# Kernel optimization log

Measured on AMD Instinct MI355X. Metric: run time of the kernel, lower is better.

Reference implementation:

```python
import jax, jax.numpy as jnp
import numpy as np

H = 4096          # hidden_size
I = 14336         # intermediate_size
SC = int(0.3 * I) # beta * I -> size of cached x_topk (4300)
HC = int(0.05 * I)# gamma * I -> helper top-k count (716)


def setup_inputs() -> dict:
    key = jax.random.key(0)
    ks = jax.random.split(key, 7)
    s = 0.02
    return {
        "x": jax.random.normal(ks[0], (1, 1, H), dtype=jnp.float32),
        "x_topk": jax.random.randint(ks[1], (SC,), 0, I, dtype=jnp.int64),
        "gate_w": jax.random.normal(ks[2], (I, H), dtype=jnp.float32) * s,
        "up_w": jax.random.normal(ks[3], (I, H), dtype=jnp.float32) * s,
        "down_w": jax.random.normal(ks[4], (H, I), dtype=jnp.float32) * s,
        "helper_w1": jax.random.normal(ks[5], (1024, H), dtype=jnp.float32) * s,
        "helper_w2": jax.random.normal(ks[6], (I, 1024), dtype=jnp.float32) * s,
    }


def reference(x, x_topk, gate_w, up_w, down_w, helper_w1, helper_w2):
    # --- sparsity predictor (SimpleLinearModel): two bias-free linears ---
    h = (x @ helper_w1.T) @ helper_w2.T                       # [1,1,I]
    up_mask_index = jax.lax.top_k(h.reshape(-1), HC)[1]       # [HC]

    # --- combine cached core indices with predicted indices, dedup ---
    combined = jnp.concatenate([x_topk.astype(jnp.int32),
                                up_mask_index.astype(jnp.int32)])  # [SC+HC]
    K = combined.shape[0]
    uniq = jnp.unique(combined, size=K, fill_value=I)         # padded with I
    valid = (uniq < I)                                        # [K] bool
    idx = jnp.where(valid, uniq, 0)                           # safe gather idx

    # --- gather weight rows/columns, reduced gated-MLP matmul ---
    gate_f = gate_w[idx]                                      # [K,H]
    up_f = up_w[idx]                                          # [K,H]
    gate_out = jnp.einsum('bsh,kh->bsk', x, gate_f)           # [1,1,K]
    up_out = jnp.einsum('bsh,kh->bsk', x, up_f)               # [1,1,K]
    tv = jax.nn.silu(gate_out) * up_out                       # act_fn = SiLU
    tv = tv * valid.astype(tv.dtype)                          # zero padded dups

    down_f = down_w[:, idx]                                   # [H,K]
    down_value = jnp.einsum('bsk,hk->bsh', tv, down_f)        # [1,1,H]
    return down_value
```

## Files before the change

### kernel.cpp

```cpp
#include <hip/hip_runtime.h>
#include <math.h>

#define H_DIM 4096
#define I_DIM 14336
#define HB_DIM 1024
#define SC_K 4300
#define HC_K 716

typedef float floatx4 __attribute__((ext_vector_type(4)));

__device__ __forceinline__ unsigned sortable(float f) {
    unsigned u = __float_as_uint(f);
    return (u & 0x80000000u) ? ~u : (u | 0x80000000u);
}

__device__ __forceinline__ floatx4 ntload4(const float* p) {
    return __builtin_nontemporal_load((const floatx4*)p);
}

__device__ __forceinline__ void compute_tv_row(const float* __restrict__ x,
                                               const float* __restrict__ gate_w,
                                               const float* __restrict__ up_w,
                                               float* __restrict__ tv, int row, int lane) {
    const float* gr = gate_w + (size_t)row * H_DIM;
    const float* ur = up_w + (size_t)row * H_DIM;
    float gs = 0.f, us = 0.f;
#pragma unroll 4
    for (int c = 0; c < H_DIM; c += 256) {
        int cc = c + lane * 4;
        float4 xv = *(const float4*)(x + cc);
        floatx4 g = ntload4(gr + cc);
        floatx4 u = ntload4(ur + cc);
        gs += g.x * xv.x + g.y * xv.y + g.z * xv.z + g.w * xv.w;
        us += u.x * xv.x + u.y * xv.y + u.z * xv.z + u.w * xv.w;
    }
#pragma unroll
    for (int o = 32; o >= 1; o >>= 1) {
        gs += __shfl_xor(gs, o);
        us += __shfl_xor(us, o);
    }
    if (lane == 0) {
        float s = gs / (1.f + expf(-gs));
        tv[row] = s * us;
    }
}

__global__ __launch_bounds__(256) void k1_h1(
    const float* __restrict__ x, const float* __restrict__ hw1,
    float* __restrict__ h1) {
    int wid = threadIdx.x >> 6, lane = threadIdx.x & 63;
    int row = blockIdx.x * 4 + wid;
    const float* mr = hw1 + (size_t)row * H_DIM;
    float s = 0.f;
#pragma unroll 4
    for (int c = 0; c < H_DIM; c += 256) {
        int cc = c + lane * 4;
        floatx4 m = ntload4(mr + cc);
        float4 v = *(const float4*)(x + cc);
        s += m.x * v.x + m.y * v.y + m.z * v.z + m.w * v.w;
    }
#pragma unroll
    for (int o = 32; o >= 1; o >>= 1) s += __shfl_xor(s, o);
    if (lane == 0) h1[row] = s;
}

__global__ __launch_bounds__(256) void k2_h_gateup(
    const float* __restrict__ h1, const float* __restrict__ hw2,
    float* __restrict__ hbuf, const int* __restrict__ x_topk,
    const float* __restrict__ x, const float* __restrict__ gate_w,
    const float* __restrict__ up_w, float* __restrict__ tv) {
    int wid = threadIdx.x >> 6, lane = threadIdx.x & 63;
    int b = blockIdx.x;
    if (b < I_DIM / 4) {
        int row = b * 4 + wid;
        const float* mr = hw2 + (size_t)row * HB_DIM;
        float s = 0.f;
#pragma unroll
        for (int c = 0; c < HB_DIM; c += 256) {
            int cc = c + lane * 4;
            floatx4 m = ntload4(mr + cc);
            float4 v = *(const float4*)(h1 + cc);
            s += m.x * v.x + m.y * v.y + m.z * v.z + m.w * v.w;
        }
#pragma unroll
        for (int o = 32; o >= 1; o >>= 1) s += __shfl_xor(s, o);
        if (lane == 0) hbuf[row] = s;
    } else {
        int row = (b - I_DIM / 4) * 4 + wid;
        bool found = false;
        for (int k = lane; k < SC_K; k += 64) found |= (x_topk[k] == row);
        if (__any(found)) compute_tv_row(x, gate_w, up_w, tv, row, lane);
    }
}

__global__ __launch_bounds__(1024) void select_kernel(
    const float* __restrict__ h, const int* __restrict__ x_topk,
    float* __restrict__ tv, int* __restrict__ rlist, int* __restrict__ rcount) {
    __shared__ unsigned hist[16][256];
    __shared__ unsigned wpart[4];
    __shared__ unsigned bitT[448], bitS[448];
    __shared__ int s_d, s_above, s_tie_cnt, s_rc;
    __shared__ int tie_idx[2048];
    int tid = threadIdx.x;
    int lane = tid & 63, wid = tid >> 6;

    unsigned key[14];
#pragma unroll
    for (int j = 0; j < 14; ++j) key[j] = sortable(h[j * 1024 + tid]);

    if (tid < 448) { bitT[tid] = 0; bitS[tid] = 0; }
    if (tid == 0) { s_tie_cnt = 0; s_rc = 0; }
    __syncthreads();

    for (int k = tid; k < SC_K; k += 1024) {
        int idx = x_topk[k];
        if ((unsigned)idx < (unsigned)I_DIM) atomicOr(&bitT[idx >> 5], 1u << (idx & 31));
    }

    unsigned prefix = 0;
    int above = 0;

    for (int p = 0; p < 4; ++p) {
        int s = 24 - 8 * p;
        {
            unsigned* hp = &hist[0][0];
            for (int i = tid; i < 4096; i += 1024) hp[i] = 0;
        }
        __syncthreads();
#pragma unroll
        for (int j = 0; j < 14; ++j) {
            unsigned u = key[j];
            bool in_sub = (p == 0) || ((u >> (s + 8)) == (prefix >> (s + 8)));
            if (in_sub) atomicAdd(&hist[wid][(u >> s) & 0xFF], 1u);
        }
        __syncthreads();
        unsigned cnt = 0, incl = 0;
        if (tid < 256) {
#pragma unroll
            for (int w = 0; w < 16; ++w) cnt += hist[w][tid];
        }
        incl = cnt;
#pragma unroll
        for (int o = 1; o < 64; o <<= 1) {
            unsigned v = __shfl_up(incl, o);
            if (lane >= o) incl += v;
        }
        if (tid < 256 && lane == 63) wpart[wid] = incl;
        __syncthreads();
        if (tid < 256) {
            unsigned add = 0;
            for (int w2 = 0; w2 < wid; ++w2) add += wpart[w2];
            incl += add;
            unsigned total = wpart[0] + wpart[1] + wpart[2] + wpart[3];
            unsigned suf = total - incl;
            unsigned needk = (unsigned)(HC_K - above);
            if (suf < needk && suf + cnt >= needk) {
                s_d = tid;
                s_above = above + (int)suf;
            }
        }
        __syncthreads();
        prefix |= ((unsigned)s_d) << s;
        above = s_above;
        __syncthreads();
    }

    unsigned T = prefix;
    int need2 = HC_K - above;

#pragma unroll
    for (int j = 0; j < 14; ++j) {
        unsigned u = key[j];
        int i = j * 1024 + tid;
        if (u > T) atomicOr(&bitS[i >> 5], 1u << (i & 31));
        else if (u == T) {
            int pp = atomicAdd(&s_tie_cnt, 1);
            if (pp < 2048) tie_idx[pp] = i;
        }
    }
    __syncthreads();
    int C = s_tie_cnt;
    if (C <= 2048) {
        for (int m = tid; m < C; m += 1024) {
            int my = tie_idx[m];
            int rank = 0;
            for (int j = 0; j < C; ++j) rank += (tie_idx[j] < my) ? 1 : 0;
            if (rank < need2) atomicOr(&bitS[my >> 5], 1u << (my & 31));
        }
    } else if (tid == 0) {
        int left = need2;
        for (int i = 0; i < I_DIM && left > 0; ++i)
            if (sortable(h[i]) == T) { atomicOr(&bitS[i >> 5], 1u << (i & 31)); --left; }
    }
    __syncthreads();

#pragma unroll
    for (int j = 0; j < 14; ++j) {
        int i = j * 1024 + tid;
        bool t = (bitT[i >> 5] >> (i & 31)) & 1u;
        bool sl = (bitS[i >> 5] >> (i & 31)) & 1u;
        if (!t) {
            if (sl) {
                int pp = atomicAdd(&s_rc, 1);
                rlist[pp] = i;
            } else {
                tv[i] = 0.f;
            }
        }
    }
    __syncthreads();
    if (tid == 0) *rcount = s_rc;
}

__global__ __launch_bounds__(256) void k3_residual(
    const float* __restrict__ x, const float* __restrict__ gate_w,
    const float* __restrict__ up_w, const int* __restrict__ rlist,
    const int* __restrict__ rcount, float* __restrict__ tv) {
    int wid = threadIdx.x >> 6, lane = threadIdx.x & 63;
    int gw = blockIdx.x * 4 + wid;
    if (gw < *rcount) compute_tv_row(x, gate_w, up_w, tv, rlist[gw], lane);
}

__global__ __launch_bounds__(256) void k4_down(
    const float* __restrict__ tv, const float* __restrict__ down_w,
    float* __restrict__ out) {
    int wid = threadIdx.x >> 6, lane = threadIdx.x & 63;
    int row = blockIdx.x * 4 + wid;
    const float* mr = down_w + (size_t)row * I_DIM;
    float s = 0.f;
#pragma unroll 4
    for (int c = 0; c < I_DIM; c += 256) {
        int cc = c + lane * 4;
        floatx4 m = ntload4(mr + cc);
        float4 v = *(const float4*)(tv + cc);
        s += m.x * v.x + m.y * v.y + m.z * v.z + m.w * v.w;
    }
#pragma unroll
    for (int o = 32; o >= 1; o >>= 1) s += __shfl_xor(s, o);
    if (lane == 0) out[row] = s;
}

extern "C" void kernel_launch(void* const* d_in, const int* in_sizes, int n_in,
                              void* d_out, int out_size, void* d_ws, size_t ws_size,
                              hipStream_t stream) {
    const float* x      = (const float*)d_in[0];
    const int*   x_topk = (const int*)d_in[1];
    const float* gate_w = (const float*)d_in[2];
    const float* up_w   = (const float*)d_in[3];
    const float* down_w = (const float*)d_in[4];
    const float* hw1    = (const float*)d_in[5];
    const float* hw2    = (const float*)d_in[6];
    float* out = (float*)d_out;

    float* ws    = (float*)d_ws;
    float* h1    = ws;
    float* hbuf  = ws + 1024;
    float* tv    = ws + 1024 + I_DIM;
    int*   rlist = (int*)(ws + 1024 + 2 * I_DIM);
    int*   rcount = rlist + 768;

    k1_h1<<<HB_DIM / 4, 256, 0, stream>>>(x, hw1, h1);
    k2_h_gateup<<<2 * (I_DIM / 4), 256, 0, stream>>>(h1, hw2, hbuf, x_topk, x,
                                                     gate_w, up_w, tv);
    select_kernel<<<1, 1024, 0, stream>>>(hbuf, x_topk, tv, rlist, rcount);
    k3_residual<<<(HC_K + 3) / 4, 256, 0, stream>>>(x, gate_w, up_w, rlist, rcount, tv);
    k4_down<<<H_DIM / 4, 256, 0, stream>>>(tv, down_w, out);
}
```

Measured before the change: 114.7 us.

## Map gate/up waves directly to cached indices instead of scanning x_topk per row

The fused helper/gate-up kernel now gives one wave to each x_topk entry and computes that row directly. Before, every one of the I rows scanned all 4300 cached indices to test membership. Fourteen extra blocks build a per-1024-row bitmap in shared memory and zero tv for rows not in the cached set. The select kernel no longer keeps a selection bitmap or does a final zeroing pass: it appends non-cached top-k rows to the residual list directly, and the histogram rows are padded to 257 entries to reduce bank conflicts. Duplicate entries in x_topk now cause the same row to be computed twice with identical results, which is redundant work but a benign race.

```diff
diff --git a/kernel.cpp b/kernel.cpp
--- a/kernel.cpp
+++ b/kernel.cpp
@@ -64,13 +64,13 @@
     if (lane == 0) h1[row] = s;
 }
 
-__global__ __launch_bounds__(256) void k2_h_gateup(
+__global__ __launch_bounds__(256) void k2_mix(
     const float* __restrict__ h1, const float* __restrict__ hw2,
     float* __restrict__ hbuf, const int* __restrict__ x_topk,
     const float* __restrict__ x, const float* __restrict__ gate_w,
     const float* __restrict__ up_w, float* __restrict__ tv) {
-    int wid = threadIdx.x >> 6, lane = threadIdx.x & 63;
     int b = blockIdx.x;
+    int wid = threadIdx.x >> 6, lane = threadIdx.x & 63;
     if (b < I_DIM / 4) {
         int row = b * 4 + wid;
         const float* mr = hw2 + (size_t)row * HB_DIM;
@@ -85,20 +85,36 @@
 #pragma unroll
         for (int o = 32; o >= 1; o >>= 1) s += __shfl_xor(s, o);
         if (lane == 0) hbuf[row] = s;
+    } else if (b < I_DIM / 4 + (SC_K + 3) / 4) {
+        int gw = (b - I_DIM / 4) * 4 + wid;
+        if (gw < SC_K) {
+            int idx = x_topk[gw];
+            if ((unsigned)idx < (unsigned)I_DIM)
+                compute_tv_row(x, gate_w, up_w, tv, idx, lane);
+        }
     } else {
-        int row = (b - I_DIM / 4) * 4 + wid;
-        bool found = false;
-        for (int k = lane; k < SC_K; k += 64) found |= (x_topk[k] == row);
-        if (__any(found)) compute_tv_row(x, gate_w, up_w, tv, row, lane);
+        int zb = b - (I_DIM / 4 + (SC_K + 3) / 4);
+        int base = zb * 1024;
+        __shared__ unsigned bits[32];
+        if (threadIdx.x < 32) bits[threadIdx.x] = 0;
+        __syncthreads();
+        for (int k = threadIdx.x; k < SC_K; k += 256) {
+            int idx = x_topk[k] - base;
+            if ((unsigned)idx < 1024u) atomicOr(&bits[idx >> 5], 1u << (idx & 31));
+        }
+        __syncthreads();
+        for (int r = threadIdx.x; r < 1024; r += 256) {
+            if (!((bits[r >> 5] >> (r & 31)) & 1u)) tv[base + r] = 0.f;
+        }
     }
 }
 
 __global__ __launch_bounds__(1024) void select_kernel(
     const float* __restrict__ h, const int* __restrict__ x_topk,
-    float* __restrict__ tv, int* __restrict__ rlist, int* __restrict__ rcount) {
-    __shared__ unsigned hist[16][256];
+    int* __restrict__ rlist, int* __restrict__ rcount) {
+    __shared__ unsigned hist[16][257];
     __shared__ unsigned wpart[4];
-    __shared__ unsigned bitT[448], bitS[448];
+    __shared__ unsigned bitT[448];
     __shared__ int s_d, s_above, s_tie_cnt, s_rc;
     __shared__ int tie_idx[2048];
     int tid = threadIdx.x;
@@ -108,7 +124,7 @@
 #pragma unroll
     for (int j = 0; j < 14; ++j) key[j] = sortable(h[j * 1024 + tid]);
 
-    if (tid < 448) { bitT[tid] = 0; bitS[tid] = 0; }
+    if (tid < 448) bitT[tid] = 0;
     if (tid == 0) { s_tie_cnt = 0; s_rc = 0; }
     __syncthreads();
 
@@ -124,7 +140,7 @@
         int s = 24 - 8 * p;
         {
             unsigned* hp = &hist[0][0];
-            for (int i = tid; i < 4096; i += 1024) hp[i] = 0;
+            for (int i = tid; i < 16 * 257; i += 1024) hp[i] = 0;
         }
         __syncthreads();
 #pragma unroll
@@ -172,8 +188,12 @@
     for (int j = 0; j < 14; ++j) {
         unsigned u = key[j];
         int i = j * 1024 + tid;
-        if (u > T) atomicOr(&bitS[i >> 5], 1u << (i & 31));
-        else if (u == T) {
+        if (u > T) {
+            if (!((bitT[i >> 5] >> (i & 31)) & 1u)) {
+                int pp = atomicAdd(&s_rc, 1);
+                rlist[pp] = i;
+            }
+        } else if (u == T) {
             int pp = atomicAdd(&s_tie_cnt, 1);
             if (pp < 2048) tie_idx[pp] = i;
         }
@@ -185,26 +205,20 @@
             int my = tie_idx[m];
             int rank = 0;
             for (int j = 0; j < C; ++j) rank += (tie_idx[j] < my) ? 1 : 0;
-            if (rank < need2) atomicOr(&bitS[my >> 5], 1u << (my & 31));
+            if (rank < need2 && !((bitT[my >> 5] >> (my & 31)) & 1u)) {
+                int pp = atomicAdd(&s_rc, 1);
+                rlist[pp] = my;
+            }
         }
     } else if (tid == 0) {
         int left = need2;
-        for (int i = 0; i < I_DIM && left > 0; ++i)
-            if (sortable(h[i]) == T) { atomicOr(&bitS[i >> 5], 1u << (i & 31)); --left; }
-    }
-    __syncthreads();
-
-#pragma unroll
-    for (int j = 0; j < 14; ++j) {
-        int i = j * 1024 + tid;
-        bool t = (bitT[i >> 5] >> (i & 31)) & 1u;
-        bool sl = (bitS[i >> 5] >> (i & 31)) & 1u;
-        if (!t) {
-            if (sl) {
-                int pp = atomicAdd(&s_rc, 1);
-                rlist[pp] = i;
-            } else {
-                tv[i] = 0.f;
+        for (int i = 0; i < I_DIM && left > 0; ++i) {
+            if (sortable(h[i]) == T) {
+                if (!((bitT[i >> 5] >> (i & 31)) & 1u)) {
+                    int pp = atomicAdd(&s_rc, 1);
+                    rlist[pp] = i;
+                }
+                --left;
             }
         }
     }
@@ -260,9 +274,9 @@
     int*   rcount = rlist + 768;
 
     k1_h1<<<HB_DIM / 4, 256, 0, stream>>>(x, hw1, h1);
-    k2_h_gateup<<<2 * (I_DIM / 4), 256, 0, stream>>>(h1, hw2, hbuf, x_topk, x,
-                                                     gate_w, up_w, tv);
-    select_kernel<<<1, 1024, 0, stream>>>(hbuf, x_topk, tv, rlist, rcount);
+    k2_mix<<<I_DIM / 4 + (SC_K + 3) / 4 + 14, 256, 0, stream>>>(
+        h1, hw2, hbuf, x_topk, x, gate_w, up_w, tv);
+    select_kernel<<<1, 1024, 0, stream>>>(hbuf, x_topk, rlist, rcount);
     k3_residual<<<(HC_K + 3) / 4, 256, 0, stream>>>(x, gate_w, up_w, rlist, rcount, tv);
     k4_down<<<H_DIM / 4, 256, 0, stream>>>(tv, down_w, out);
 }
```

Result: faster. 102.1 us (-11.0%).
